# Optimization experiments

Hardware: AMD Instinct MI355X
Metric: run time of the kernel (lower is better)

The kernel has to match this reference:

```python
import jax, jax.numpy as jnp
import numpy as np

IN_V = 16
OUT_V = 16
HS = 64
INCR = 2
METRIC = jnp.array([1.0, -1.0, -1.0, -1.0], dtype=jnp.float32)


def setup_inputs() -> dict:
    key = jax.random.key(0)
    ks = jax.random.split(key, 9)
    B, N = 64, 1024
    vectors = jax.random.normal(ks[0], (B, N, IN_V, 4), dtype=jnp.float32)
    scalars = jax.random.normal(ks[1], (B, N, HS), dtype=jnp.float32)
    # kaiming-uniform-ish init scale for [out, in] weights
    def w(k, o, i):
        bound = 1.0 / np.sqrt(i)
        return jax.random.uniform(k, (o, i), jnp.float32, -bound, bound)
    Wq = w(ks[2], IN_V * INCR, IN_V)
    Wk = w(ks[3], IN_V * INCR, IN_V)
    Wv = w(ks[4], OUT_V, IN_V)  # exp() applied in forward (EquiLinearTimelike)
    Wq_s = w(ks[5], HS, HS)
    Wk_s = w(ks[6], HS, HS)
    bq_s = jax.random.uniform(ks[7], (HS,), jnp.float32, -1 / np.sqrt(HS), 1 / np.sqrt(HS))
    bk_s = jax.random.uniform(ks[8], (HS,), jnp.float32, -1 / np.sqrt(HS), 1 / np.sqrt(HS))
    return {"vectors": vectors, "scalars": scalars, "Wq": Wq, "Wq_s": Wq_s,
            "bq_s": bq_s, "Wk": Wk, "Wk_s": Wk_s, "bk_s": bk_s, "Wv": Wv}


def reference(vectors, scalars, Wq, Wq_s, bq_s, Wk, Wk_s, bk_s, Wv):
    B, N = vectors.shape[:2]
    # Lorentz squared norm: t^2 - x^2 - y^2 - z^2 over last axis -> [B,N,IN_V,1]
    norm = jnp.einsum('bnik,k->bni', vectors * vectors, METRIC)[..., None]
    vecs = vectors / jnp.sqrt(jnp.clip(jnp.abs(norm), 1e-5))
    # Q/K vector projections [B,N,IN_V*INCR,4] and scalar projections [B,N,HS]
    q_v = jnp.einsum('ij,bnjk->bnik', Wq, vecs)
    k_v = jnp.einsum('ij,bnjk->bnik', Wk, vecs)
    q_s = scalars @ Wq_s.T + bq_s
    k_s = scalars @ Wk_s.T + bk_s
    # embed: flatten vectors (K gets metric factor) and concat scalars
    q = jnp.concatenate([q_v.reshape(B, N, -1), q_s], axis=-1)
    k = jnp.concatenate([(k_v * METRIC).reshape(B, N, -1), k_s], axis=-1)
    # V: positive-weight (timelike) projection, flatten -> [B,N,OUT_V*4]
    v = jnp.einsum('ij,bnjk->bnik', jnp.exp(Wv), vecs).reshape(B, N, -1)
    # scaled dot-product attention over the particle axis
    scale = 1.0 / jnp.sqrt(jnp.asarray(q.shape[-1], q.dtype))
    scores = jnp.einsum('bqd,bkd->bqk', q, k) * scale
    attn = jax.nn.softmax(scores, axis=-1)
    out = jnp.einsum('bqk,bkd->bqd', attn, v)
    return out.reshape(B, N, -1, 4)
```

## Files before the change

kernel.cpp:

```cpp
#include <hip/hip_runtime.h>
#include <math.h>

typedef float f32x16 __attribute__((ext_vector_type(16)));
typedef short bf16x8 __attribute__((ext_vector_type(8)));
typedef short bf16x4 __attribute__((ext_vector_type(4)));
typedef unsigned short u16;
typedef unsigned int u32;

#define MFMA32(a, b, c) __builtin_amdgcn_mfma_f32_32x32x16_bf16(a, b, c, 0, 0, 0)

__device__ __forceinline__ u16 f2bf(float x) {
    u32 u = __float_as_uint(x);
    u += 0x7FFFu + ((u >> 16) & 1u);
    return (u16)(u >> 16);
}
__device__ __forceinline__ float bf2f(u16 h) {
    return __uint_as_float(((u32)h) << 16);
}

__global__ __launch_bounds__(256) void g_kernel(
    const float* __restrict__ Wq, const float* __restrict__ Wk,
    const float* __restrict__ Wv,
    u16* __restrict__ gmh, u16* __restrict__ gml,
    u16* __restrict__ mvh, u16* __restrict__ mvl)
{
    const int bk = blockIdx.x;
    const int base = ((bk & 3) * 256 + threadIdx.x) * 4;
    if (bk < 4) {
#pragma unroll
        for (int i = 0; i < 4; ++i) {
            int e = base + i;
            int f = e >> 6, fp = e & 63;
            int c = f & 3, cp = fp & 3, j = f >> 2, jp = fp >> 2;
            float val = 0.f;
            if (c == cp) {
                float a0 = 0.f, a1 = 0.f;
#pragma unroll 8
                for (int ff = 0; ff < 32; ff += 2) {
                    a0 = fmaf(Wq[ff * 16 + j],       Wk[ff * 16 + jp],       a0);
                    a1 = fmaf(Wq[(ff + 1) * 16 + j], Wk[(ff + 1) * 16 + jp], a1);
                }
                val = (a0 + a1) * ((c == 0) ? 1.f : -1.f);
            }
            u16 h = f2bf(val);
            gmh[e] = h; gml[e] = f2bf(val - bf2f(h));
        }
    } else {
#pragma unroll
        for (int i = 0; i < 4; ++i) {
            int e = base + i;
            int f = e >> 6, fp = e & 63;
            float val = ((f & 3) == (fp & 3)) ? expf(Wv[(f >> 2) * 16 + (fp >> 2)]) : 0.f;
            u16 h = f2bf(val);
            mvh[e] = h; mvl[e] = f2bf(val - bf2f(h));
        }
    }
}

__global__ __launch_bounds__(256) void prep_kernel(
    const float* __restrict__ vectors, const float* __restrict__ scalars,
    const float* __restrict__ Wq_s, const float* __restrict__ bq_s,
    const float* __restrict__ Wk_s, const float* __restrict__ bk_s,
    const u16* __restrict__ gmh, const u16* __restrict__ gml,
    const u16* __restrict__ mvh, const u16* __restrict__ mvl,
    u16* __restrict__ qh, u16* __restrict__ ql,
    u16* __restrict__ kh, u16* __restrict__ kl,
    u16* __restrict__ vth)
{
    const int t = threadIdx.x;
    const int w = t >> 6;
    const int lane = t & 63;
    const int l31 = lane & 31, g = lane >> 5;
    const int b = blockIdx.x >> 5;
    const int n0 = (blockIdx.x & 31) << 5;
    const long tok0 = (long)b * 1024 + n0;
    const float SC = 0.07216878364870323f;

    if (w == 1 || w == 2) {
        bf16x8 Ah[4], Al[4];
        const float* vrow = vectors + (tok0 + l31) * 64 + g * 8;
#pragma unroll
        for (int kk = 0; kk < 4; ++kk) {
            float4 x0 = *(const float4*)(vrow + kk * 16);
            float4 x1 = *(const float4*)(vrow + kk * 16 + 4);
            float nr0 = x0.x * x0.x - x0.y * x0.y - x0.z * x0.z - x0.w * x0.w;
            float iv0 = 1.0f / sqrtf(fmaxf(fabsf(nr0), 1e-5f));
            float nr1 = x1.x * x1.x - x1.y * x1.y - x1.z * x1.z - x1.w * x1.w;
            float iv1 = 1.0f / sqrtf(fmaxf(fabsf(nr1), 1e-5f));
            float xs[8] = {x0.x * iv0, x0.y * iv0, x0.z * iv0, x0.w * iv0,
                           x1.x * iv1, x1.y * iv1, x1.z * iv1, x1.w * iv1};
#pragma unroll
            for (int e = 0; e < 8; ++e) {
                u16 h = f2bf(xs[e]);
                Ah[kk][e] = (short)h;
                Al[kk][e] = (short)f2bf(xs[e] - bf2f(h));
            }
        }

        const u16* bhp = (w == 1) ? gmh : mvh;
        const u16* blp = (w == 1) ? gml : mvl;
#pragma unroll
        for (int tile = 0; tile < 2; ++tile) {
            const int fs = tile * 32 + l31;
            const u16* bh = bhp + fs * 64 + g * 8;
            const u16* bl = blp + fs * 64 + g * 8;
            f32x16 acc;
#pragma unroll
            for (int r = 0; r < 16; ++r) acc[r] = 0.f;
#pragma unroll
            for (int kk = 0; kk < 4; ++kk) {
                bf16x8 Bh = *(const bf16x8*)(bh + kk * 16);
                bf16x8 Bl = *(const bf16x8*)(bl + kk * 16);
                acc = MFMA32(Ah[kk], Bh, acc);
                acc = MFMA32(Al[kk], Bh, acc);
                acc = MFMA32(Ah[kk], Bl, acc);
            }
            if (w == 1) {
#pragma unroll
                for (int reg = 0; reg < 16; ++reg) {
                    int trow = (reg & 3) + 8 * (reg >> 2) + 4 * g;
                    float val = acc[reg];
                    u16 h = f2bf(val);
                    kh[(tok0 + trow) * 128 + fs] = h;
                    kl[(tok0 + trow) * 64 + fs] = f2bf(val - bf2f(h));
                }
            } else {
#pragma unroll
                for (int reg = 0; reg < 16; ++reg) {
                    int trow = (reg & 3) + 8 * (reg >> 2) + 4 * g;
                    vth[((long)b * 64 + fs) * 1024 + n0 + trow] = f2bf(acc[reg]);
                }
            }
        }
    } else {
        if (w == 0) {
            const float* vrow = vectors + (tok0 + l31) * 64 + g * 8;
#pragma unroll
            for (int kk = 0; kk < 4; ++kk) {
                float4 x0 = *(const float4*)(vrow + kk * 16);
                float4 x1 = *(const float4*)(vrow + kk * 16 + 4);
                float nr0 = x0.x * x0.x - x0.y * x0.y - x0.z * x0.z - x0.w * x0.w;
                float iv0 = SC / sqrtf(fmaxf(fabsf(nr0), 1e-5f));
                float nr1 = x1.x * x1.x - x1.y * x1.y - x1.z * x1.z - x1.w * x1.w;
                float iv1 = SC / sqrtf(fmaxf(fabsf(nr1), 1e-5f));
                float xs[8] = {x0.x * iv0, x0.y * iv0, x0.z * iv0, x0.w * iv0,
                               x1.x * iv1, x1.y * iv1, x1.z * iv1, x1.w * iv1};
                u16 hh[8], ll[8];
#pragma unroll
                for (int e = 0; e < 8; ++e) {
                    hh[e] = f2bf(xs[e]);
                    ll[e] = f2bf(xs[e] - bf2f(hh[e]));
                }
                *(int4*)(qh + (tok0 + l31) * 128 + kk * 16 + g * 8) = *(int4*)hh;
                *(int4*)(ql + (tok0 + l31) * 64 + kk * 16 + g * 8) = *(int4*)ll;
            }
        }
        const int isq = (w == 0);
        bf16x8 Ah[4];
        const float* xrow = scalars + (tok0 + l31) * 64 + g * 8;
#pragma unroll
        for (int kk = 0; kk < 4; ++kk) {
            float4 x0 = *(const float4*)(xrow + kk * 16);
            float4 x1 = *(const float4*)(xrow + kk * 16 + 4);
            float xs[8] = {x0.x, x0.y, x0.z, x0.w, x1.x, x1.y, x1.z, x1.w};
#pragma unroll
            for (int e = 0; e < 8; ++e) Ah[kk][e] = (short)f2bf(xs[e]);
        }
        const float sc = isq ? SC : 1.f;
        u16* oh = isq ? qh : kh;
#pragma unroll
        for (int ft = 0; ft < 2; ++ft) {
            const int fs = (ft << 5) + l31;
            const float* wrow = (isq ? Wq_s : Wk_s) + fs * 64 + g * 8;
            f32x16 acc;
#pragma unroll
            for (int r = 0; r < 16; ++r) acc[r] = 0.f;
#pragma unroll
            for (int kk = 0; kk < 4; ++kk) {
                float4 w0_ = *(const float4*)(wrow + kk * 16);
                float4 w1_ = *(const float4*)(wrow + kk * 16 + 4);
                float ws_[8] = {w0_.x, w0_.y, w0_.z, w0_.w, w1_.x, w1_.y, w1_.z, w1_.w};
                bf16x8 Bh;
#pragma unroll
                for (int e = 0; e < 8; ++e) Bh[e] = (short)f2bf(ws_[e]);
                acc = MFMA32(Ah[kk], Bh, acc);
            }
            const float bias = (isq ? bq_s : bk_s)[fs];
#pragma unroll
            for (int reg = 0; reg < 16; ++reg) {
                int trow = (reg & 3) + 8 * (reg >> 2) + 4 * g;
                oh[(tok0 + trow) * 128 + 64 + fs] = f2bf((acc[reg] + bias) * sc);
            }
        }
    }
}

__global__ __launch_bounds__(256) void attn_kernel(
    const u16* __restrict__ qh, const u16* __restrict__ ql,
    const u16* __restrict__ kh, const u16* __restrict__ kl,
    const u16* __restrict__ vth, float* __restrict__ po,
    float2* __restrict__ pml)
{
    __shared__ u16 KH[2 * 32 * 128];
    __shared__ u16 KL[2 * 32 * 64];
    __shared__ u16 VH[2 * 64 * 40];

    const int t = threadIdx.x;
    const int lane = t & 63;
    const int w = t >> 6;
    const int l31 = lane & 31, g = lane >> 5;

    const int bid = blockIdx.x;
    const int xcd = bid & 7;
    const int idx = bid >> 3;
    const int b = xcd * 8 + (idx >> 4);
    const int qt = (idx >> 1) & 7;
    const int half = idx & 1;
    const int kv0 = half << 9;

    const int qi = qt * 128 + w * 32 + l31;
    const long qtok = (long)b * 1024 + qi;

    bf16x8 Qh[8], Qlv[4];
    {
        const u16* qhp = qh + qtok * 128 + g * 8;
        const u16* qlp = ql + qtok * 64 + g * 8;
#pragma unroll
        for (int c = 0; c < 8; ++c) Qh[c] = *(const bf16x8*)(qhp + c * 16);
#pragma unroll
        for (int c = 0; c < 4; ++c) Qlv[c] = *(const bf16x8*)(qlp + c * 16);
    }

    const int krow = t >> 3, ku = t & 7;
    const u16* khg = kh + ((long)b * 1024 + kv0 + krow) * 128 + ku * 16;
    const u16* klg = kl + ((long)b * 1024 + kv0 + krow) * 64 + ku * 8;
    const int kd0 = krow * 128 + (((ku << 1)    ) ^ (krow & 15)) * 8;
    const int kd1 = krow * 128 + (((ku << 1) + 1) ^ (krow & 15)) * 8;
    const int kdl = krow * 64 + (ku ^ (krow & 7)) * 8;
    const int vdv = t >> 2, vq4 = t & 3;
    const u16* vhg = vth + ((long)b * 64 + vdv) * 1024 + kv0 + vq4 * 8;
    u16* vdst = VH + vdv * 40 + vq4 * 8;

    int4 rk0, rk1, rl0, rv0;

#define LOADT(kt) do { \
        const u16* p1 = khg + (long)(kt) * 128; \
        rk0 = *(const int4*)(p1); rk1 = *(const int4*)(p1 + 8); \
        rl0 = *(const int4*)(klg + (long)(kt) * 64); \
        rv0 = *(const int4*)(vhg + (kt)); \
    } while (0)

#define WRITET(buf) do { \
        u16* d = KH + (buf) * 4096; \
        *(int4*)(d + kd0) = rk0; *(int4*)(d + kd1) = rk1; \
        *(int4*)(KL + (buf) * 2048 + kdl) = rl0; \
        *(int4*)(vdst + (buf) * 2560) = rv0; \
    } while (0)

    f32x16 o0, o1;
#pragma unroll
    for (int r = 0; r < 16; ++r) { o0[r] = 0.f; o1[r] = 0.f; }
    float m_run = -1e30f, l_run = 0.f;

    LOADT(0);
    WRITET(0);
    __syncthreads();

    for (int it = 0; it < 16; ++it) {
        const int cb = it & 1;
        if (it < 15) LOADT((it + 1) * 32);

        f32x16 sA, sB;
#pragma unroll
        for (int r = 0; r < 16; ++r) { sA[r] = 0.f; sB[r] = 0.f; }
        const u16* kbh = KH + cb * 4096 + l31 * 128;
        const u16* kbl = KL + cb * 2048 + l31 * 64;
        const int rs = l31 & 15, rs7 = l31 & 7;
        __builtin_amdgcn_s_setprio(1);
#pragma unroll
        for (int c = 0; c < 4; ++c) {
            bf16x8 fh = *(const bf16x8*)(kbh + ((g + 2 * c) ^ rs) * 8);
            bf16x8 fl = *(const bf16x8*)(kbl + ((g + 2 * c) ^ rs7) * 8);
            sA = MFMA32(fh, Qh[c], sA);
            sB = MFMA32(fl, Qh[c], sB);
            sB = MFMA32(fh, Qlv[c], sB);
        }
#pragma unroll
        for (int c = 4; c < 8; ++c) {
            bf16x8 fh = *(const bf16x8*)(kbh + ((g + 2 * c) ^ rs) * 8);
            sA = MFMA32(fh, Qh[c], sA);
        }
        __builtin_amdgcn_s_setprio(0);

        float s[16];
#pragma unroll
        for (int r = 0; r < 16; ++r) s[r] = sA[r] + sB[r];
        float mt = s[0];
#pragma unroll
        for (int r = 1; r < 16; ++r) mt = fmaxf(mt, s[r]);
        mt = fmaxf(mt, __shfl_xor(mt, 32));
        if (!__all(mt - m_run <= 8.f)) {
            float mn = fmaxf(m_run, mt);
            float corr = __expf(m_run - mn);
            l_run *= corr;
#pragma unroll
            for (int r = 0; r < 16; ++r) { o0[r] *= corr; o1[r] *= corr; }
            m_run = mn;
        }
        float ps = 0.f;
#pragma unroll
        for (int r = 0; r < 16; ++r) { s[r] = __expf(s[r] - m_run); ps += s[r]; }
        ps += __shfl_xor(ps, 32);
        l_run += ps;

        bf16x8 ph0, ph1;
#pragma unroll
        for (int e = 0; e < 8; ++e) {
            ph0[e] = (short)f2bf(s[e]);
            ph1[e] = (short)f2bf(s[8 + e]);
        }

        const u16* vb = VH + cb * 2560;
        bf16x8 v00, v01, v10, v11;
        {
            const u16* p00 = vb + l31 * 40 + g * 4;
            const u16* p10 = vb + (32 + l31) * 40 + g * 4;
            bf16x4 a0 = *(const bf16x4*)(p00);      bf16x4 a1 = *(const bf16x4*)(p00 + 8);
            bf16x4 b0 = *(const bf16x4*)(p00 + 16); bf16x4 b1 = *(const bf16x4*)(p00 + 24);
            bf16x4 c0 = *(const bf16x4*)(p10);      bf16x4 c1 = *(const bf16x4*)(p10 + 8);
            bf16x4 d0 = *(const bf16x4*)(p10 + 16); bf16x4 d1 = *(const bf16x4*)(p10 + 24);
            v00 = __builtin_shufflevector(a0, a1, 0, 1, 2, 3, 4, 5, 6, 7);
            v01 = __builtin_shufflevector(b0, b1, 0, 1, 2, 3, 4, 5, 6, 7);
            v10 = __builtin_shufflevector(c0, c1, 0, 1, 2, 3, 4, 5, 6, 7);
            v11 = __builtin_shufflevector(d0, d1, 0, 1, 2, 3, 4, 5, 6, 7);
        }

        __builtin_amdgcn_s_setprio(1);
        o0 = MFMA32(v00, ph0, o0);
        o0 = MFMA32(v01, ph1, o0);
        o1 = MFMA32(v10, ph0, o1);
        o1 = MFMA32(v11, ph1, o1);
        __builtin_amdgcn_s_setprio(0);

        if (it < 15) WRITET(cb ^ 1);
        __syncthreads();
    }

    float* poA = po + (((long)half * 64 + b) * 1024 + qi) * 64;
#pragma unroll
    for (int sg = 0; sg < 4; ++sg) {
        *(float4*)(poA + sg * 8 + g * 4) = make_float4(
            o0[4*sg+0], o0[4*sg+1], o0[4*sg+2], o0[4*sg+3]);
        *(float4*)(poA + 32 + sg * 8 + g * 4) = make_float4(
            o1[4*sg+0], o1[4*sg+1], o1[4*sg+2], o1[4*sg+3]);
    }
    if (g == 0) {
        pml[((long)half * 64 + b) * 1024 + qi] = make_float2(m_run, l_run);
    }
#undef LOADT
#undef WRITET
}

__global__ __launch_bounds__(256) void merge_kernel(
    const float* __restrict__ po, const float2* __restrict__ pml,
    float* __restrict__ out)
{
    const int idx = blockIdx.x * 256 + threadIdx.x;
    const int q = idx >> 2;
    const int part = idx & 3;
    float2 a = pml[q];
    float2 c = pml[65536 + q];
    float m = fmaxf(a.x, c.x);
    float w0 = __expf(a.x - m), w1 = __expf(c.x - m);
    float inv = 1.0f / (w0 * a.y + w1 * c.y);
    const float4* o0 = (const float4*)(po + (long)q * 64 + part * 16);
    const float4* o1 = (const float4*)(po + 4194304 + (long)q * 64 + part * 16);
    float4* op = (float4*)(out + (long)q * 64 + part * 16);
#pragma unroll
    for (int j = 0; j < 4; ++j) {
        float4 x = o0[j], y = o1[j];
        op[j] = make_float4((w0 * x.x + w1 * y.x) * inv,
                            (w0 * x.y + w1 * y.y) * inv,
                            (w0 * x.z + w1 * y.z) * inv,
                            (w0 * x.w + w1 * y.w) * inv);
    }
}

extern "C" void kernel_launch(void* const* d_in, const int* in_sizes, int n_in,
                              void* d_out, int out_size, void* d_ws, size_t ws_size,
                              hipStream_t stream) {
    const float* vectors = (const float*)d_in[0];
    const float* scalars = (const float*)d_in[1];
    const float* Wq   = (const float*)d_in[2];
    const float* Wq_s = (const float*)d_in[3];
    const float* bq_s = (const float*)d_in[4];
    const float* Wk   = (const float*)d_in[5];
    const float* Wk_s = (const float*)d_in[6];
    const float* bk_s = (const float*)d_in[7];
    const float* Wv   = (const float*)d_in[8];
    float* o = (float*)d_out;

    u16* qh  = (u16*)d_ws;
    u16* ql  = qh + 8388608;
    u16* kh  = ql + 4194304;
    u16* kl  = kh + 8388608;
    u16* vth = kl + 4194304;
    float* po = (float*)(vth + 4194304);
    float2* pml = (float2*)(po + 8388608);
    u16* gmh = (u16*)(pml + 131072);
    u16* gml = gmh + 4096;
    u16* mvh = gml + 4096;
    u16* mvl = mvh + 4096;

    g_kernel<<<8, 256, 0, stream>>>(Wq, Wk, Wv, gmh, gml, mvh, mvl);
    prep_kernel<<<2048, 256, 0, stream>>>(vectors, scalars, Wq_s, bq_s,
                                          Wk_s, bk_s, gmh, gml, mvh, mvl,
                                          qh, ql, kh, kl, vth);
    attn_kernel<<<1024, 256, 0, stream>>>(qh, ql, kh, kl, vth, po, pml);
    merge_kernel<<<1024, 256, 0, stream>>>(po, pml, o);
}
```

Baseline: 107.1 us.

## Stage K/V tiles via direct global-to-LDS loads and store partials as bf16

Replaces register-staged K/V tile loads plus LDS writes with global_load_lds direct copies into a swizzled, unpadded LDS layout, waiting on vmcnt before each barrier. Merges the two score accumulators into one MFMA chain, and writes partial attention outputs as bf16 instead of fp32, halving merge traffic. Aims to cut VGPR pressure, LDS write instructions and memory bandwidth, but adds bf16 rounding to partial outputs and serialises the score MFMA dependency chain.

```diff
diff --git a/kernel.cpp b/kernel.cpp
--- a/kernel.cpp
+++ b/kernel.cpp
@@ -16,6 +16,11 @@
 }
 __device__ __forceinline__ float bf2f(u16 h) {
     return __uint_as_float(((u32)h) << 16);
+}
+__device__ __forceinline__ void gload16(const void* g, void* l) {
+    __builtin_amdgcn_global_load_lds(
+        (const __attribute__((address_space(1))) unsigned int*)g,
+        (__attribute__((address_space(3))) unsigned int*)l, 16, 0, 0);
 }
 
 __global__ __launch_bounds__(256) void g_kernel(
@@ -198,12 +203,12 @@
 __global__ __launch_bounds__(256) void attn_kernel(
     const u16* __restrict__ qh, const u16* __restrict__ ql,
     const u16* __restrict__ kh, const u16* __restrict__ kl,
-    const u16* __restrict__ vth, float* __restrict__ po,
+    const u16* __restrict__ vth, u16* __restrict__ pob,
     float2* __restrict__ pml)
 {
     __shared__ u16 KH[2 * 32 * 128];
     __shared__ u16 KL[2 * 32 * 64];
-    __shared__ u16 VH[2 * 64 * 40];
+    __shared__ u16 VH[2 * 64 * 32];
 
     const int t = threadIdx.x;
     const int lane = t & 63;
@@ -231,30 +236,24 @@
         for (int c = 0; c < 4; ++c) Qlv[c] = *(const bf16x8*)(qlp + c * 16);
     }
 
-    const int krow = t >> 3, ku = t & 7;
-    const u16* khg = kh + ((long)b * 1024 + kv0 + krow) * 128 + ku * 16;
-    const u16* klg = kl + ((long)b * 1024 + kv0 + krow) * 64 + ku * 8;
-    const int kd0 = krow * 128 + (((ku << 1)    ) ^ (krow & 15)) * 8;
-    const int kd1 = krow * 128 + (((ku << 1) + 1) ^ (krow & 15)) * 8;
-    const int kdl = krow * 64 + (ku ^ (krow & 7)) * 8;
-    const int vdv = t >> 2, vq4 = t & 3;
-    const u16* vhg = vth + ((long)b * 64 + vdv) * 1024 + kv0 + vq4 * 8;
-    u16* vdst = VH + vdv * 40 + vq4 * 8;
-
-    int4 rk0, rk1, rl0, rv0;
-
-#define LOADT(kt) do { \
-        const u16* p1 = khg + (long)(kt) * 128; \
-        rk0 = *(const int4*)(p1); rk1 = *(const int4*)(p1 + 8); \
-        rl0 = *(const int4*)(klg + (long)(kt) * 64); \
-        rv0 = *(const int4*)(vhg + (kt)); \
-    } while (0)
-
-#define WRITET(buf) do { \
-        u16* d = KH + (buf) * 4096; \
-        *(int4*)(d + kd0) = rk0; *(int4*)(d + kd1) = rk1; \
-        *(int4*)(KL + (buf) * 2048 + kdl) = rl0; \
-        *(int4*)(vdst + (buf) * 2560) = rv0; \
+    const int r0 = 8 * w + (lane >> 4);
+    const int r1 = r0 + 4;
+    const int su0 = (lane & 15) ^ (r0 & 15);
+    const int su1 = (lane & 15) ^ (r1 & 15);
+    const u16* kh0 = kh + ((long)b * 1024 + kv0 + r0) * 128 + su0 * 8;
+    const u16* kh1 = kh + ((long)b * 1024 + kv0 + r1) * 128 + su1 * 8;
+    const int rl_ = 8 * w + (lane >> 3);
+    const int sul = (lane & 7) ^ (rl_ & 7);
+    const u16* kl0 = kl + ((long)b * 1024 + kv0 + rl_) * 64 + sul * 8;
+    const int dv_ = 16 * w + (lane >> 2);
+    const int suv = (lane & 3) ^ (dv_ & 3);
+    const u16* vh0 = vth + ((long)b * 64 + dv_) * 1024 + kv0 + suv * 8;
+
+#define STAGE(kt, bf) do { \
+        gload16(kh0 + (long)(kt) * 128, KH + (bf) * 4096 + w * 1024); \
+        gload16(kh1 + (long)(kt) * 128, KH + (bf) * 4096 + w * 1024 + 512); \
+        gload16(kl0 + (long)(kt) * 64,  KL + (bf) * 2048 + w * 512); \
+        gload16(vh0 + (kt),             VH + (bf) * 2048 + w * 512); \
     } while (0)
 
     f32x16 o0, o1;
@@ -262,17 +261,17 @@
     for (int r = 0; r < 16; ++r) { o0[r] = 0.f; o1[r] = 0.f; }
     float m_run = -1e30f, l_run = 0.f;
 
-    LOADT(0);
-    WRITET(0);
+    STAGE(0, 0);
+    asm volatile("s_waitcnt vmcnt(0)" ::: "memory");
     __syncthreads();
 
     for (int it = 0; it < 16; ++it) {
         const int cb = it & 1;
-        if (it < 15) LOADT((it + 1) * 32);
-
-        f32x16 sA, sB;
-#pragma unroll
-        for (int r = 0; r < 16; ++r) { sA[r] = 0.f; sB[r] = 0.f; }
+        if (it < 15) STAGE((it + 1) * 32, cb ^ 1);
+
+        f32x16 sA;
+#pragma unroll
+        for (int r = 0; r < 16; ++r) sA[r] = 0.f;
         const u16* kbh = KH + cb * 4096 + l31 * 128;
         const u16* kbl = KL + cb * 2048 + l31 * 64;
         const int rs = l31 & 15, rs7 = l31 & 7;
@@ -282,8 +281,8 @@
             bf16x8 fh = *(const bf16x8*)(kbh + ((g + 2 * c) ^ rs) * 8);
             bf16x8 fl = *(const bf16x8*)(kbl + ((g + 2 * c) ^ rs7) * 8);
             sA = MFMA32(fh, Qh[c], sA);
-            sB = MFMA32(fl, Qh[c], sB);
-            sB = MFMA32(fh, Qlv[c], sB);
+            sA = MFMA32(fl, Qh[c], sA);
+            sA = MFMA32(fh, Qlv[c], sA);
         }
 #pragma unroll
         for (int c = 4; c < 8; ++c) {
@@ -294,7 +293,7 @@
 
         float s[16];
 #pragma unroll
-        for (int r = 0; r < 16; ++r) s[r] = sA[r] + sB[r];
+        for (int r = 0; r < 16; ++r) s[r] = sA[r];
         float mt = s[0];
 #pragma unroll
         for (int r = 1; r < 16; ++r) mt = fmaxf(mt, s[r]);
@@ -320,15 +319,20 @@
             ph1[e] = (short)f2bf(s[8 + e]);
         }
 
-        const u16* vb = VH + cb * 2560;
+        const u16* vb = VH + cb * 2048;
+        const int rsw = l31 & 3;
         bf16x8 v00, v01, v10, v11;
         {
-            const u16* p00 = vb + l31 * 40 + g * 4;
-            const u16* p10 = vb + (32 + l31) * 40 + g * 4;
-            bf16x4 a0 = *(const bf16x4*)(p00);      bf16x4 a1 = *(const bf16x4*)(p00 + 8);
-            bf16x4 b0 = *(const bf16x4*)(p00 + 16); bf16x4 b1 = *(const bf16x4*)(p00 + 24);
-            bf16x4 c0 = *(const bf16x4*)(p10);      bf16x4 c1 = *(const bf16x4*)(p10 + 8);
-            bf16x4 d0 = *(const bf16x4*)(p10 + 16); bf16x4 d1 = *(const bf16x4*)(p10 + 24);
+            const u16* p00 = vb + l31 * 32 + g * 4;
+            const u16* p10 = vb + (32 + l31) * 32 + g * 4;
+            bf16x4 a0 = *(const bf16x4*)(p00 + ((0 ^ rsw) * 8));
+            bf16x4 a1 = *(const bf16x4*)(p00 + ((1 ^ rsw) * 8));
+            bf16x4 b0 = *(const bf16x4*)(p00 + ((2 ^ rsw) * 8));
+            bf16x4 b1 = *(const bf16x4*)(p00 + ((3 ^ rsw) * 8));
+            bf16x4 c0 = *(const bf16x4*)(p10 + ((0 ^ rsw) * 8));
+            bf16x4 c1 = *(const bf16x4*)(p10 + ((1 ^ rsw) * 8));
+            bf16x4 d0 = *(const bf16x4*)(p10 + ((2 ^ rsw) * 8));
+            bf16x4 d1 = *(const bf16x4*)(p10 + ((3 ^ rsw) * 8));
             v00 = __builtin_shufflevector(a0, a1, 0, 1, 2, 3, 4, 5, 6, 7);
             v01 = __builtin_shufflevector(b0, b1, 0, 1, 2, 3, 4, 5, 6, 7);
             v10 = __builtin_shufflevector(c0, c1, 0, 1, 2, 3, 4, 5, 6, 7);
@@ -342,27 +346,28 @@
         o1 = MFMA32(v11, ph1, o1);
         __builtin_amdgcn_s_setprio(0);
 
-        if (it < 15) WRITET(cb ^ 1);
+        asm volatile("s_waitcnt vmcnt(0)" ::: "memory");
         __syncthreads();
     }
 
-    float* poA = po + (((long)half * 64 + b) * 1024 + qi) * 64;
+    u16* poA = pob + (long)half * 4194304 + qtok * 64;
 #pragma unroll
     for (int sg = 0; sg < 4; ++sg) {
-        *(float4*)(poA + sg * 8 + g * 4) = make_float4(
-            o0[4*sg+0], o0[4*sg+1], o0[4*sg+2], o0[4*sg+3]);
-        *(float4*)(poA + 32 + sg * 8 + g * 4) = make_float4(
-            o1[4*sg+0], o1[4*sg+1], o1[4*sg+2], o1[4*sg+3]);
+        u32 pk0 = (u32)f2bf(o0[4 * sg + 0]) | ((u32)f2bf(o0[4 * sg + 1]) << 16);
+        u32 pk1 = (u32)f2bf(o0[4 * sg + 2]) | ((u32)f2bf(o0[4 * sg + 3]) << 16);
+        *(int2*)(poA + sg * 8 + g * 4) = make_int2((int)pk0, (int)pk1);
+        u32 pk2 = (u32)f2bf(o1[4 * sg + 0]) | ((u32)f2bf(o1[4 * sg + 1]) << 16);
+        u32 pk3 = (u32)f2bf(o1[4 * sg + 2]) | ((u32)f2bf(o1[4 * sg + 3]) << 16);
+        *(int2*)(poA + 32 + sg * 8 + g * 4) = make_int2((int)pk2, (int)pk3);
     }
     if (g == 0) {
         pml[((long)half * 64 + b) * 1024 + qi] = make_float2(m_run, l_run);
     }
-#undef LOADT
-#undef WRITET
+#undef STAGE
 }
 
 __global__ __launch_bounds__(256) void merge_kernel(
-    const float* __restrict__ po, const float2* __restrict__ pml,
+    const u16* __restrict__ pob, const float2* __restrict__ pml,
     float* __restrict__ out)
 {
     const int idx = blockIdx.x * 256 + threadIdx.x;
@@ -373,16 +378,22 @@
     float m = fmaxf(a.x, c.x);
     float w0 = __expf(a.x - m), w1 = __expf(c.x - m);
     float inv = 1.0f / (w0 * a.y + w1 * c.y);
-    const float4* o0 = (const float4*)(po + (long)q * 64 + part * 16);
-    const float4* o1 = (const float4*)(po + 4194304 + (long)q * 64 + part * 16);
+    const u16* p0 = pob + (long)q * 64 + part * 16;
+    const u16* p1 = p0 + 4194304;
+    u16 va[16], vb[16];
+    *(int4*)&va[0] = *(const int4*)p0;
+    *(int4*)&va[8] = *(const int4*)(p0 + 8);
+    *(int4*)&vb[0] = *(const int4*)p1;
+    *(int4*)&vb[8] = *(const int4*)(p1 + 8);
     float4* op = (float4*)(out + (long)q * 64 + part * 16);
 #pragma unroll
     for (int j = 0; j < 4; ++j) {
-        float4 x = o0[j], y = o1[j];
-        op[j] = make_float4((w0 * x.x + w1 * y.x) * inv,
-                            (w0 * x.y + w1 * y.y) * inv,
-                            (w0 * x.z + w1 * y.z) * inv,
-                            (w0 * x.w + w1 * y.w) * inv);
+        float4 o4;
+        o4.x = (w0 * bf2f(va[j * 4 + 0]) + w1 * bf2f(vb[j * 4 + 0])) * inv;
+        o4.y = (w0 * bf2f(va[j * 4 + 1]) + w1 * bf2f(vb[j * 4 + 1])) * inv;
+        o4.z = (w0 * bf2f(va[j * 4 + 2]) + w1 * bf2f(vb[j * 4 + 2])) * inv;
+        o4.w = (w0 * bf2f(va[j * 4 + 3]) + w1 * bf2f(vb[j * 4 + 3])) * inv;
+        op[j] = o4;
     }
 }
 
@@ -405,8 +416,8 @@
     u16* kh  = ql + 4194304;
     u16* kl  = kh + 8388608;
     u16* vth = kl + 4194304;
-    float* po = (float*)(vth + 4194304);
-    float2* pml = (float2*)(po + 8388608);
+    u16* pob = vth + 4194304;
+    float2* pml = (float2*)(pob + 8388608);
     u16* gmh = (u16*)(pml + 131072);
     u16* gml = gmh + 4096;
     u16* mvh = gml + 4096;
@@ -416,6 +427,6 @@
     prep_kernel<<<2048, 256, 0, stream>>>(vectors, scalars, Wq_s, bq_s,
                                           Wk_s, bk_s, gmh, gml, mvh, mvl,
                                           qh, ql, kh, kl, vth);
-    attn_kernel<<<1024, 256, 0, stream>>>(qh, ql, kh, kl, vth, po, pml);
-    merge_kernel<<<1024, 256, 0, stream>>>(po, pml, o);
-}
+    attn_kernel<<<1024, 256, 0, stream>>>(qh, ql, kh, kl, vth, pob, pml);
+    merge_kernel<<<1024, 256, 0, stream>>>(pob, pml, o);
+}
```

New measurement: 111.3 us. 1.04x slower.
